# Kernel optimization log

Hardware: AMD Instinct MI355X
Metric: run time of the kernel (lower is better)

Reference implementation:

```python
import jax, jax.numpy as jnp
import numpy as np

N_NODES = 50000
N_EDGES = 600000
N_GRAPHS = 512
D = 128          # in_channels == hidden_channels
L = 4            # num_layers (total GINConv count)
N_CLASSES = 10
BN_EPS = 1e-5


def setup_inputs() -> dict:
    key = jax.random.key(0)
    ks = jax.random.split(key, 12)
    x = jax.random.normal(ks[0], (N_NODES, D), dtype=jnp.float32)
    edge_index = jax.random.randint(ks[1], (2, N_EDGES), 0, N_NODES, dtype=jnp.int64)
    batch = jnp.sort(jax.random.randint(ks[2], (N_NODES,), 0, N_GRAPHS, dtype=jnp.int64))
    s = 1.0 / np.sqrt(D)
    W1 = jax.random.uniform(ks[3], (L, D, D), jnp.float32, -s, s)
    b1 = jax.random.uniform(ks[4], (L, D), jnp.float32, -s, s)
    W2 = jax.random.uniform(ks[5], (L, D, D), jnp.float32, -s, s)
    b2 = jax.random.uniform(ks[6], (L, D), jnp.float32, -s, s)
    eps = jnp.zeros((L,), jnp.float32)            # train_eps=True, init 0
    gamma = jnp.ones((L, D), jnp.float32)
    beta = jnp.zeros((L, D), jnp.float32)
    sl = 1.0 / np.sqrt(D * L)
    Wlin = jax.random.uniform(ks[7], (D * L, N_CLASSES), jnp.float32, -sl, sl)
    blin = jax.random.uniform(ks[8], (N_CLASSES,), jnp.float32, -sl, sl)
    return {"x": x, "edge_index": edge_index, "batch": batch,
            "W1": W1, "b1": b1, "W2": W2, "b2": b2, "eps": eps,
            "gamma": gamma, "beta": beta, "Wlin": Wlin, "blin": blin}


def reference(x, edge_index, batch, W1, b1, W2, b2, eps, gamma, beta, Wlin, blin):
    src, dst = edge_index[0], edge_index[1]
    h = x
    pools = []
    for l in range(L):
        # GINConv: sum-aggregate neighbor features at dst, add (1+eps)*self
        agg = jax.ops.segment_sum(h[src], dst, num_segments=N_NODES)
        z = (1.0 + eps[l]) * h + agg
        # 2-layer MLP
        z = jnp.maximum(z @ W1[l] + b1[l], 0.0) @ W2[l] + b2[l]
        # BatchNorm1d (training mode: batch stats, biased variance)
        mean = jnp.mean(z, axis=0)
        var = jnp.mean(jnp.square(z - mean), axis=0)
        z = (z - mean) * jax.lax.rsqrt(var + BN_EPS) * gamma[l] + beta[l]
        h = jnp.maximum(z, 0.0)
        # global_add_pool per graph
        pools.append(jax.ops.segment_sum(h, batch, num_segments=N_GRAPHS))
    x_cat = jnp.concatenate(pools, axis=1)  # [N_GRAPHS, D*L]
    return x_cat @ Wlin + blin              # dropout = identity (eval)
```

## Files before the change

### kernel.cpp

```cpp
#include <hip/hip_runtime.h>

#define N_NODES 50000
#define N_EDGES 600000
#define N_GRAPHS 512
#define DIM 128
#define NLAYERS 4
#define NCLASSES 10
#define KPS 136

typedef __attribute__((ext_vector_type(8))) short short8;
typedef __attribute__((ext_vector_type(4))) float f32x4;

union Frag { short8 s; uint4 u; };

__device__ inline unsigned short f2bf(float v) {
    union { float f; unsigned u; } c; c.f = v;
    unsigned u = c.u;
    u += 0x7FFFu + ((u >> 16) & 1u);
    return (unsigned short)(u >> 16);
}
__device__ inline float bfu_lo(unsigned u) {
    union { float f; unsigned x; } c; c.x = u << 16; return c.f;
}
__device__ inline float bfu_hi(unsigned u) {
    union { float f; unsigned x; } c; c.x = u & 0xFFFF0000u; return c.f;
}
__device__ inline void addRow(float* acc, const uint4& v) {
    acc[0] += bfu_lo(v.x); acc[1] += bfu_hi(v.x);
    acc[2] += bfu_lo(v.y); acc[3] += bfu_hi(v.y);
    acc[4] += bfu_lo(v.z); acc[5] += bfu_hi(v.z);
    acc[6] += bfu_lo(v.w); acc[7] += bfu_hi(v.w);
}

__global__ __launch_bounds__(256) void hist_kernel(
    const int* __restrict__ dst, int* __restrict__ deg)
{
    int e = blockIdx.x * 256 + threadIdx.x;
    if (e >= N_EDGES) return;
    atomicAdd(&deg[dst[e]], 1);
}

__global__ __launch_bounds__(256) void scan1_kernel(
    const int* __restrict__ deg, int* __restrict__ bsum)
{
    __shared__ int red[256];
    int t = threadIdx.x;
    int i4 = blockIdx.x * 256 + t;
    int s = 0;
    if (i4 < 12500) {
        int4 v = ((const int4*)deg)[i4];
        s = v.x + v.y + v.z + v.w;
    }
    red[t] = s;
    __syncthreads();
    for (int off = 128; off > 0; off >>= 1) {
        if (t < off) red[t] += red[t + off];
        __syncthreads();
    }
    if (t == 0) bsum[blockIdx.x] = red[0];
}

__global__ __launch_bounds__(64) void scan2_kernel(int* __restrict__ bsum)
{
    __shared__ int sh[64];
    int t = threadIdx.x;
    sh[t] = (t < 49) ? bsum[t] : 0;
    __syncthreads();
    if (t == 0) {
        int run = 0;
        for (int i = 0; i < 49; i++) { int v = sh[i]; sh[i] = run; run += v; }
    }
    __syncthreads();
    if (t < 49) bsum[t] = sh[t];
}

__global__ __launch_bounds__(256) void scan3_kernel(
    const int* __restrict__ deg, const int* __restrict__ bsum,
    int* __restrict__ rowptr, int* __restrict__ cursor)
{
    __shared__ int red[256];
    int t = threadIdx.x;
    int i4 = blockIdx.x * 256 + t;
    int4 v = {0, 0, 0, 0};
    if (i4 < 12500) v = ((const int4*)deg)[i4];
    int s = v.x + v.y + v.z + v.w;
    red[t] = s;
    __syncthreads();
    for (int off = 1; off < 256; off <<= 1) {
        int val = (t >= off) ? red[t - off] : 0;
        __syncthreads();
        red[t] += val;
        __syncthreads();
    }
    int run = bsum[blockIdx.x] + (t ? red[t - 1] : 0);
    if (i4 < 12500) {
        int4 rp;
        rp.x = run; run += v.x;
        rp.y = run; run += v.y;
        rp.z = run; run += v.z;
        rp.w = run; run += v.w;
        ((int4*)rowptr)[i4] = rp;
        ((int4*)cursor)[i4] = rp;
    }
    if (blockIdx.x == 0 && t == 0) rowptr[N_NODES] = N_EDGES;
}

__global__ __launch_bounds__(256) void fill_kernel(
    const int* __restrict__ src, const int* __restrict__ dst,
    int* __restrict__ cursor, int* __restrict__ csr)
{
    int e = blockIdx.x * 256 + threadIdx.x;
    if (e >= N_EDGES) return;
    int p = atomicAdd(&cursor[dst[e]], 1);
    csr[p] = src[e];
}

__global__ __launch_bounds__(256) void prep_kernel(
    const int* __restrict__ batch, int* __restrict__ gstart,
    const float* __restrict__ x, unsigned int* __restrict__ xb,
    const float* __restrict__ W1, const float* __restrict__ W2,
    unsigned short* __restrict__ whi, float* __restrict__ stats)
{
    int b = blockIdx.x;
    int t = threadIdx.x;
    if (b < 196) {
        int n = b * 256 + t;
        if (n >= N_NODES) return;
        int bb = batch[n];
        int bp = (n == 0) ? -1 : batch[n - 1];
        for (int g = bp + 1; g <= bb; g++) gstart[g] = n;
        if (n == N_NODES - 1)
            for (int g = bb + 1; g <= N_GRAPHS; g++) gstart[g] = N_NODES;
    } else if (b < 6446) {
        int idx = (b - 196) * 256 + t;
        if (idx >= N_NODES * 32) return;
        float4 v = ((const float4*)x)[idx];
        uint2 o;
        o.x = (unsigned)f2bf(v.x) | ((unsigned)f2bf(v.y) << 16);
        o.y = (unsigned)f2bf(v.z) | ((unsigned)f2bf(v.w) << 16);
        ((uint2*)xb)[idx] = o;
    } else if (b < 6958) {
        int idx = (b - 6446) * 256 + t;
        int f   = idx & 16383;
        int w01 = (idx >> 14) & 1;
        int l   = idx >> 15;
        int j    = f & 7;
        int lane = (f >> 3) & 63;
        int cg   = (f >> 9) & 7;
        int ks   = f >> 12;
        int k = ks * 32 + (lane >> 4) * 8 + j;
        int n = cg * 16 + (lane & 15);
        const float* W = (w01 == 0 ? W1 : W2) + (size_t)l * 16384;
        whi[idx] = f2bf(W[k * 128 + n]);
    } else {
        #pragma unroll
        for (int i = 0; i < 4; i++) stats[i * 256 + t] = 0.f;
    }
}

__global__ __launch_bounds__(256) void gin_layer_kernel(
    const unsigned int* __restrict__ hb,
    const int* __restrict__ rowptr, const int* __restrict__ csr,
    const float* __restrict__ epsP,
    unsigned short* __restrict__ z,
    const unsigned short* __restrict__ whi,
    const float* __restrict__ b1, const float* __restrict__ b2,
    float* __restrict__ stats)
{
    __shared__ unsigned short tpk[64 * KPS];
    __shared__ float sums[1024];
    __shared__ float sqs[1024];

    const int t = threadIdx.x;
    const int lane = t & 63;
    const int w = t >> 6;
    const int wr = w & 1, wc = w >> 1;
    const int l15 = lane & 15, quad = lane >> 4;
    const int base = blockIdx.x * 64;

    {
        const int m = t >> 2;
        const int c = t & 3;
        const int n = base + m;
        const uint4* hb4 = (const uint4*)hb;
        float acc[32];
        #pragma unroll
        for (int i = 0; i < 32; i++) acc[i] = 0.f;
        if (n < N_NODES) {
            const float e1 = 1.0f + epsP[0];
            const uint4* self = hb4 + (size_t)n * 16 + c;
            #pragma unroll
            for (int j = 0; j < 4; j++) {
                uint4 v = self[j * 4];
                float* a = acc + j * 8;
                a[0] = e1 * bfu_lo(v.x); a[1] = e1 * bfu_hi(v.x);
                a[2] = e1 * bfu_lo(v.y); a[3] = e1 * bfu_hi(v.y);
                a[4] = e1 * bfu_lo(v.z); a[5] = e1 * bfu_hi(v.z);
                a[6] = e1 * bfu_lo(v.w); a[7] = e1 * bfu_hi(v.w);
            }
            int beg = rowptr[n], end = rowptr[n + 1];
            int e = beg;
            if (e + 3 < end) {
                int s0 = csr[e], s1 = csr[e + 1], s2 = csr[e + 2], s3 = csr[e + 3];
                while (true) {
                    const uint4* r0 = hb4 + (size_t)s0 * 16 + c;
                    const uint4* r1 = hb4 + (size_t)s1 * 16 + c;
                    const uint4* r2 = hb4 + (size_t)s2 * 16 + c;
                    const uint4* r3 = hb4 + (size_t)s3 * 16 + c;
                    uint4 v00 = r0[0], v01 = r0[4], v02 = r0[8], v03 = r0[12];
                    uint4 v10 = r1[0], v11 = r1[4], v12 = r1[8], v13 = r1[12];
                    uint4 v20 = r2[0], v21 = r2[4], v22 = r2[8], v23 = r2[12];
                    uint4 v30 = r3[0], v31 = r3[4], v32 = r3[8], v33 = r3[12];
                    int en = e + 4;
                    bool more = (en + 3 < end);
                    if (more) {
                        s0 = csr[en]; s1 = csr[en + 1];
                        s2 = csr[en + 2]; s3 = csr[en + 3];
                    }
                    addRow(acc + 0, v00); addRow(acc + 8, v01); addRow(acc + 16, v02); addRow(acc + 24, v03);
                    addRow(acc + 0, v10); addRow(acc + 8, v11); addRow(acc + 16, v12); addRow(acc + 24, v13);
                    addRow(acc + 0, v20); addRow(acc + 8, v21); addRow(acc + 16, v22); addRow(acc + 24, v23);
                    addRow(acc + 0, v30); addRow(acc + 8, v31); addRow(acc + 16, v32); addRow(acc + 24, v33);
                    e = en;
                    if (!more) break;
                }
            }
            for (; e < end; e++) {
                int s0 = csr[e];
                const uint4* r0 = hb4 + (size_t)s0 * 16 + c;
                uint4 a0 = r0[0], a1 = r0[4], a2 = r0[8], a3 = r0[12];
                addRow(acc + 0, a0);  addRow(acc + 8, a1);
                addRow(acc + 16, a2); addRow(acc + 24, a3);
            }
        }
        #pragma unroll
        for (int j = 0; j < 4; j++) {
            union { short8 s; unsigned short u[8]; } pk;
            #pragma unroll
            for (int i = 0; i < 8; i++) pk.u[i] = f2bf(acc[j * 8 + i]);
            *((short8*)&tpk[m * KPS + j * 32 + c * 8]) = pk.s;
        }
    }
    __syncthreads();

    f32x4 acc[2][4];
    #pragma unroll
    for (int s = 0; s < 2; s++)
        #pragma unroll
        for (int i = 0; i < 4; i++) acc[s][i] = (f32x4){0.f, 0.f, 0.f, 0.f};

    const int arow0 = (32 * wr + l15) * KPS;
    const int arow1 = arow0 + 16 * KPS;

    #pragma unroll
    for (int kh = 0; kh < 2; kh++) {
        Frag bf[2][4];
        short8 a0[2], a1[2];
        #pragma unroll
        for (int kk = 0; kk < 2; kk++) {
            int ks = kh * 2 + kk;
            #pragma unroll
            for (int i = 0; i < 4; i++) {
                size_t woff = (size_t)(((ks * 8 + wc * 4 + i) * 64 + lane) * 8);
                bf[kk][i].s = *((const short8*)&whi[woff]);
            }
            a0[kk] = *((const short8*)&tpk[arow0 + ks * 32 + quad * 8]);
            a1[kk] = *((const short8*)&tpk[arow1 + ks * 32 + quad * 8]);
        }
        #pragma unroll
        for (int kk = 0; kk < 2; kk++) {
            #pragma unroll
            for (int i = 0; i < 4; i++) {
                acc[0][i] = __builtin_amdgcn_mfma_f32_16x16x32_bf16(a0[kk], bf[kk][i].s, acc[0][i], 0, 0, 0);
                acc[1][i] = __builtin_amdgcn_mfma_f32_16x16x32_bf16(a1[kk], bf[kk][i].s, acc[1][i], 0, 0, 0);
            }
        }
    }
    __syncthreads();

    #pragma unroll
    for (int i = 0; i < 4; i++) {
        int col = wc * 64 + i * 16 + l15;
        float bb = b1[col];
        #pragma unroll
        for (int s = 0; s < 2; s++) {
            #pragma unroll
            for (int r = 0; r < 4; r++) {
                int m = 32 * wr + 16 * s + quad * 4 + r;
                float v = fmaxf(acc[s][i][r] + bb, 0.f);
                tpk[m * KPS + col] = f2bf(v);
            }
            acc[s][i] = (f32x4){0.f, 0.f, 0.f, 0.f};
        }
    }
    __syncthreads();

    const unsigned short* w2 = whi + 16384;
    #pragma unroll
    for (int kh = 0; kh < 2; kh++) {
        Frag bf[2][4];
        short8 a0[2], a1[2];
        #pragma unroll
        for (int kk = 0; kk < 2; kk++) {
            int ks = kh * 2 + kk;
            #pragma unroll
            for (int i = 0; i < 4; i++) {
                size_t woff = (size_t)(((ks * 8 + wc * 4 + i) * 64 + lane) * 8);
                bf[kk][i].s = *((const short8*)&w2[woff]);
            }
            a0[kk] = *((const short8*)&tpk[arow0 + ks * 32 + quad * 8]);
            a1[kk] = *((const short8*)&tpk[arow1 + ks * 32 + quad * 8]);
        }
        #pragma unroll
        for (int kk = 0; kk < 2; kk++) {
            #pragma unroll
            for (int i = 0; i < 4; i++) {
                acc[0][i] = __builtin_amdgcn_mfma_f32_16x16x32_bf16(a0[kk], bf[kk][i].s, acc[0][i], 0, 0, 0);
                acc[1][i] = __builtin_amdgcn_mfma_f32_16x16x32_bf16(a1[kk], bf[kk][i].s, acc[1][i], 0, 0, 0);
            }
        }
    }
    __syncthreads();

    {
        float colsum[4], colsq[4];
        #pragma unroll
        for (int i = 0; i < 4; i++) {
            int col = wc * 64 + i * 16 + l15;
            float bb = b2[col];
            float su = 0.f, q2 = 0.f;
            #pragma unroll
            for (int s = 0; s < 2; s++) {
                #pragma unroll
                for (int r = 0; r < 4; r++) {
                    int m = 32 * wr + 16 * s + quad * 4 + r;
                    int n = base + m;
                    float v = acc[s][i][r] + bb;
                    tpk[m * KPS + col] = f2bf(v);
                    if (n < N_NODES) { su += v; q2 += v * v; }
                }
            }
            colsum[i] = su; colsq[i] = q2;
        }
        #pragma unroll
        for (int i = 0; i < 4; i++) {
            sums[(w * 4 + i) * 64 + lane] = colsum[i];
            sqs [(w * 4 + i) * 64 + lane] = colsq[i];
        }
    }
    __syncthreads();

    {
        int m2 = t >> 2, c2 = t & 3;
        int n2 = base + m2;
        if (n2 < N_NODES) {
            const uint4* srcp = (const uint4*)(tpk + m2 * KPS);
            uint4* dstp = (uint4*)z + (size_t)n2 * 16;
            #pragma unroll
            for (int j = 0; j < 4; j++) dstp[j * 4 + c2] = srcp[j * 4 + c2];
        }
    }
    if (t < 128) {
        int c = t;
        int wcc = c >> 6, ci = (c >> 4) & 3, cl = c & 15;
        float s = 0.f, q2 = 0.f;
        #pragma unroll
        for (int wrr = 0; wrr < 2; wrr++) {
            int ww = wcc * 2 + wrr;
            #pragma unroll
            for (int u = 0; u < 4; u++) {
                int ln = cl + u * 16;
                s  += sums[(ww * 4 + ci) * 64 + ln];
                q2 += sqs [(ww * 4 + ci) * 64 + ln];
            }
        }
        unsafeAtomicAdd(&stats[c], s);
        unsafeAtomicAdd(&stats[128 + c], q2);
    }
}

__global__ __launch_bounds__(256) void bnpool_kernel(
    const unsigned int* __restrict__ z, const float* __restrict__ stats,
    const float* __restrict__ gamma, const float* __restrict__ beta,
    const int* __restrict__ gstart, unsigned int* __restrict__ hout,
    float* __restrict__ pools, int layer)
{
    __shared__ float red[8][128];
    const int g = blockIdx.x;
    const int t = threadIdx.x;
    const int q = t & 31, r = t >> 5;
    const int beg = gstart[g], end = gstart[g + 1];

    float4 s  = ((const float4*)stats)[q];
    float4 sq = ((const float4*)stats)[32 + q];
    float4 gm = ((const float4*)gamma)[q];
    float4 bt = ((const float4*)beta)[q];
    const float invN = 1.0f / (float)N_NODES;
    float m, vr;
    float4 scl, sh;
    m = s.x * invN; vr = sq.x * invN - m * m; scl.x = gm.x * rsqrtf(vr + 1e-5f); sh.x = bt.x - m * scl.x;
    m = s.y * invN; vr = sq.y * invN - m * m; scl.y = gm.y * rsqrtf(vr + 1e-5f); sh.y = bt.y - m * scl.y;
    m = s.z * invN; vr = sq.z * invN - m * m; scl.z = gm.z * rsqrtf(vr + 1e-5f); sh.z = bt.z - m * scl.z;
    m = s.w * invN; vr = sq.w * invN - m * m; scl.w = gm.w * rsqrtf(vr + 1e-5f); sh.w = bt.w - m * scl.w;

    float4 acc = {0.f, 0.f, 0.f, 0.f};
    for (int n = beg + r; n < end; n += 8) {
        uint2 zp = ((const uint2*)z)[(size_t)n * 32 + q];
        float4 hv;
        hv.x = fmaxf(bfu_lo(zp.x) * scl.x + sh.x, 0.f);
        hv.y = fmaxf(bfu_hi(zp.x) * scl.y + sh.y, 0.f);
        hv.z = fmaxf(bfu_lo(zp.y) * scl.z + sh.z, 0.f);
        hv.w = fmaxf(bfu_hi(zp.y) * scl.w + sh.w, 0.f);
        uint2 p;
        p.x = (unsigned)f2bf(hv.x) | ((unsigned)f2bf(hv.y) << 16);
        p.y = (unsigned)f2bf(hv.z) | ((unsigned)f2bf(hv.w) << 16);
        ((uint2*)hout)[(size_t)n * 32 + q] = p;
        acc.x += hv.x; acc.y += hv.y; acc.z += hv.z; acc.w += hv.w;
    }
    red[r][q * 4 + 0] = acc.x;
    red[r][q * 4 + 1] = acc.y;
    red[r][q * 4 + 2] = acc.z;
    red[r][q * 4 + 3] = acc.w;
    __syncthreads();
    if (t < 128) {
        float sm = 0.f;
        #pragma unroll
        for (int rr = 0; rr < 8; rr++) sm += red[rr][t];
        pools[(size_t)g * (DIM * NLAYERS) + (size_t)layer * DIM + t] = sm;
    }
}

__global__ __launch_bounds__(64) void final_kernel(
    const float* __restrict__ pools, const float* __restrict__ Wlin,
    const float* __restrict__ blin, float* __restrict__ out)
{
    int g = blockIdx.x;
    int lane = threadIdx.x;
    const float* xr = pools + (size_t)g * (DIM * NLAYERS);
    float a[NCLASSES];
    #pragma unroll
    for (int o = 0; o < NCLASSES; o++) a[o] = 0.f;
    for (int kk = 0; kk < DIM * NLAYERS; kk += 64) {
        float xv = xr[kk + lane];
        const float* wr = Wlin + (size_t)(kk + lane) * NCLASSES;
        #pragma unroll
        for (int o = 0; o < NCLASSES; o++) a[o] += xv * wr[o];
    }
    #pragma unroll
    for (int o = 0; o < NCLASSES; o++) {
        float v = a[o];
        #pragma unroll
        for (int off = 32; off > 0; off >>= 1) v += __shfl_down(v, off, 64);
        if (lane == 0) out[(size_t)g * NCLASSES + o] = v + blin[o];
    }
}

extern "C" void kernel_launch(void* const* d_in, const int* in_sizes, int n_in,
                              void* d_out, int out_size, void* d_ws, size_t ws_size,
                              hipStream_t stream)
{
    const float* x     = (const float*)d_in[0];
    const int*   src   = (const int*)d_in[1];
    const int*   dst   = ((const int*)d_in[1]) + N_EDGES;
    const int*   batch = (const int*)d_in[2];
    const float* W1    = (const float*)d_in[3];
    const float* b1    = (const float*)d_in[4];
    const float* W2    = (const float*)d_in[5];
    const float* b2    = (const float*)d_in[6];
    const float* eps   = (const float*)d_in[7];
    const float* gamma = (const float*)d_in[8];
    const float* beta  = (const float*)d_in[9];
    const float* Wlin  = (const float*)d_in[10];
    const float* blin  = (const float*)d_in[11];
    float* out = (float*)d_out;

    char* ws = (char*)d_ws;
    const size_t FEATH = (size_t)N_NODES * DIM * sizeof(unsigned short);
    size_t off = 0;
    unsigned int* buf_h = (unsigned int*)(ws + off); off += FEATH;
    unsigned short* buf_z = (unsigned short*)(ws + off); off += FEATH;
    float* pools  = (float*)(ws + off); off += (size_t)N_GRAPHS * DIM * NLAYERS * sizeof(float);
    float* stats  = (float*)(ws + off); off += (size_t)NLAYERS * 256 * sizeof(float);
    int*   deg    = (int*)(ws + off);   off += (size_t)N_NODES * sizeof(int);
    int*   rowptr = (int*)(ws + off);   off += (size_t)(N_NODES + 1) * sizeof(int) + 12;
    int*   csr    = (int*)(ws + off);   off += (size_t)N_EDGES * sizeof(int);
    int*   gstart = (int*)(ws + off);   off += 2064;
    int*   bsum   = (int*)(ws + off);   off += 208;
    unsigned short* whi = (unsigned short*)(ws + off); off += (size_t)NLAYERS * 2 * 16384 * 2;

    hipMemsetAsync(deg, 0, (size_t)N_NODES * sizeof(int), stream);

    hist_kernel<<<(N_EDGES + 255) / 256, 256, 0, stream>>>(dst, deg);
    scan1_kernel<<<49, 256, 0, stream>>>(deg, bsum);
    scan2_kernel<<<1, 64, 0, stream>>>(bsum);
    scan3_kernel<<<49, 256, 0, stream>>>(deg, bsum, rowptr, deg );
    fill_kernel<<<(N_EDGES + 255) / 256, 256, 0, stream>>>(src, dst, deg, csr);
    prep_kernel<<<6959, 256, 0, stream>>>(batch, gstart, x, buf_h,
                                          W1, W2, whi, stats);

    for (int l = 0; l < NLAYERS; l++) {
        gin_layer_kernel<<<(N_NODES + 63) / 64, 256, 0, stream>>>(
            buf_h, rowptr, csr, eps + l, buf_z,
            whi + (size_t)l * 32768,
            b1 + (size_t)l * DIM, b2 + (size_t)l * DIM,
            stats + (size_t)l * 256);
        bnpool_kernel<<<N_GRAPHS, 256, 0, stream>>>(
            (const unsigned int*)buf_z, stats + (size_t)l * 256,
            gamma + (size_t)l * DIM, beta + (size_t)l * DIM,
            gstart, buf_h, pools, l);
    }
    final_kernel<<<N_GRAPHS, 64, 0, stream>>>(pools, Wlin, blin, out);
}
```

Before: 406.8 us.

## Fuse BatchNorm+ReLU and pooling into next GIN layer's gather, merge head

```diff
diff --git a/kernel.cpp b/kernel.cpp
--- a/kernel.cpp
+++ b/kernel.cpp
@@ -30,6 +30,26 @@
     acc[2] += bfu_lo(v.y); acc[3] += bfu_hi(v.y);
     acc[4] += bfu_lo(v.z); acc[5] += bfu_hi(v.z);
     acc[6] += bfu_lo(v.w); acc[7] += bfu_hi(v.w);
+}
+__device__ inline void bnRow(float* h, const uint4& v, const unsigned* cf) {
+    h[0] = fmaxf(bfu_lo(v.x) * bfu_hi(cf[0]) + bfu_lo(cf[0]), 0.f);
+    h[1] = fmaxf(bfu_hi(v.x) * bfu_hi(cf[1]) + bfu_lo(cf[1]), 0.f);
+    h[2] = fmaxf(bfu_lo(v.y) * bfu_hi(cf[2]) + bfu_lo(cf[2]), 0.f);
+    h[3] = fmaxf(bfu_hi(v.y) * bfu_hi(cf[3]) + bfu_lo(cf[3]), 0.f);
+    h[4] = fmaxf(bfu_lo(v.z) * bfu_hi(cf[4]) + bfu_lo(cf[4]), 0.f);
+    h[5] = fmaxf(bfu_hi(v.z) * bfu_hi(cf[5]) + bfu_lo(cf[5]), 0.f);
+    h[6] = fmaxf(bfu_lo(v.w) * bfu_hi(cf[6]) + bfu_lo(cf[6]), 0.f);
+    h[7] = fmaxf(bfu_hi(v.w) * bfu_hi(cf[7]) + bfu_lo(cf[7]), 0.f);
+}
+template<int MODE>
+__device__ inline void addRowM(float* a, const uint4& v, const unsigned* cf) {
+    if constexpr (MODE) {
+        float h[8]; bnRow(h, v, cf);
+        a[0] += h[0]; a[1] += h[1]; a[2] += h[2]; a[3] += h[3];
+        a[4] += h[4]; a[5] += h[5]; a[6] += h[6]; a[7] += h[7];
+    } else {
+        addRow(a, v);
+    }
 }
 
 __global__ __launch_bounds__(256) void hist_kernel(
@@ -119,7 +139,8 @@
     const int* __restrict__ batch, int* __restrict__ gstart,
     const float* __restrict__ x, unsigned int* __restrict__ xb,
     const float* __restrict__ W1, const float* __restrict__ W2,
-    unsigned short* __restrict__ whi, float* __restrict__ stats)
+    unsigned short* __restrict__ whi, float* __restrict__ stats,
+    float* __restrict__ pools)
 {
     int b = blockIdx.x;
     int t = threadIdx.x;
@@ -152,24 +173,32 @@
         int n = cg * 16 + (lane & 15);
         const float* W = (w01 == 0 ? W1 : W2) + (size_t)l * 16384;
         whi[idx] = f2bf(W[k * 128 + n]);
+    } else if (b == 6958) {
+        #pragma unroll
+        for (int i = 0; i < 4; i++) stats[i * 256 + t] = 0.f;
     } else {
-        #pragma unroll
-        for (int i = 0; i < 4; i++) stats[i * 256 + t] = 0.f;
-    }
-}
-
+        int idx = (b - 6959) * 256 + t;
+        pools[idx] = 0.f;
+    }
+}
+
+template<int MODE>
 __global__ __launch_bounds__(256) void gin_layer_kernel(
-    const unsigned int* __restrict__ hb,
+    const unsigned int* __restrict__ zin,
     const int* __restrict__ rowptr, const int* __restrict__ csr,
     const float* __restrict__ epsP,
-    unsigned short* __restrict__ z,
+    unsigned short* __restrict__ zout,
     const unsigned short* __restrict__ whi,
     const float* __restrict__ b1, const float* __restrict__ b2,
-    float* __restrict__ stats)
+    float* __restrict__ stats,
+    const float* __restrict__ statsP,
+    const float* __restrict__ gammaP, const float* __restrict__ betaP,
+    const int* __restrict__ batch, float* __restrict__ pools, int lm1)
 {
     __shared__ unsigned short tpk[64 * KPS];
     __shared__ float sums[1024];
     __shared__ float sqs[1024];
+    __shared__ float pool_lds[8][128];
 
     const int t = threadIdx.x;
     const int lane = t & 63;
@@ -178,25 +207,74 @@
     const int l15 = lane & 15, quad = lane >> 4;
     const int base = blockIdx.x * 64;
 
+    if constexpr (MODE) {
+        ((float*)pool_lds)[t]       = 0.f;
+        ((float*)pool_lds)[256 + t] = 0.f;
+        ((float*)pool_lds)[512 + t] = 0.f;
+        ((float*)pool_lds)[768 + t] = 0.f;
+        __syncthreads();
+    }
+
     {
         const int m = t >> 2;
         const int c = t & 3;
         const int n = base + m;
-        const uint4* hb4 = (const uint4*)hb;
+        const uint4* hb4 = (const uint4*)zin;
         float acc[32];
+        unsigned cf[32];
         #pragma unroll
         for (int i = 0; i < 32; i++) acc[i] = 0.f;
+        if constexpr (MODE) {
+            const float invN = 1.0f / (float)N_NODES;
+            #pragma unroll
+            for (int j = 0; j < 4; j++) {
+                int cb = 32 * j + 8 * c;
+                #pragma unroll
+                for (int k = 0; k < 8; k++) {
+                    float mean = statsP[cb + k] * invN;
+                    float var  = statsP[128 + cb + k] * invN - mean * mean;
+                    float scl  = gammaP[cb + k] * rsqrtf(var + 1e-5f);
+                    float shv  = betaP[cb + k] - mean * scl;
+                    cf[j * 8 + k] = ((unsigned)f2bf(scl) << 16) | (unsigned)f2bf(shv);
+                }
+            }
+        }
         if (n < N_NODES) {
             const float e1 = 1.0f + epsP[0];
             const uint4* self = hb4 + (size_t)n * 16 + c;
-            #pragma unroll
-            for (int j = 0; j < 4; j++) {
-                uint4 v = self[j * 4];
-                float* a = acc + j * 8;
-                a[0] = e1 * bfu_lo(v.x); a[1] = e1 * bfu_hi(v.x);
-                a[2] = e1 * bfu_lo(v.y); a[3] = e1 * bfu_hi(v.y);
-                a[4] = e1 * bfu_lo(v.z); a[5] = e1 * bfu_hi(v.z);
-                a[6] = e1 * bfu_lo(v.w); a[7] = e1 * bfu_hi(v.w);
+            if constexpr (MODE) {
+                int g = batch[n];
+                int slot = g - batch[base];
+                #pragma unroll
+                for (int j = 0; j < 4; j++) {
+                    uint4 v = self[j * 4];
+                    float h[8];
+                    bnRow(h, v, cf + j * 8);
+                    int cb = 32 * j + 8 * c;
+                    if (slot < 8) {
+                        #pragma unroll
+                        for (int k = 0; k < 8; k++)
+                            atomicAdd(&pool_lds[slot][cb + k], h[k]);
+                    } else {
+                        #pragma unroll
+                        for (int k = 0; k < 8; k++)
+                            unsafeAtomicAdd(&pools[(size_t)g * (DIM * NLAYERS)
+                                                   + (size_t)lm1 * DIM + cb + k], h[k]);
+                    }
+                    float* a = acc + j * 8;
+                    #pragma unroll
+                    for (int k = 0; k < 8; k++) a[k] = e1 * h[k];
+                }
+            } else {
+                #pragma unroll
+                for (int j = 0; j < 4; j++) {
+                    uint4 v = self[j * 4];
+                    float* a = acc + j * 8;
+                    a[0] = e1 * bfu_lo(v.x); a[1] = e1 * bfu_hi(v.x);
+                    a[2] = e1 * bfu_lo(v.y); a[3] = e1 * bfu_hi(v.y);
+                    a[4] = e1 * bfu_lo(v.z); a[5] = e1 * bfu_hi(v.z);
+                    a[6] = e1 * bfu_lo(v.w); a[7] = e1 * bfu_hi(v.w);
+                }
             }
             int beg = rowptr[n], end = rowptr[n + 1];
             int e = beg;
@@ -217,10 +295,14 @@
                         s0 = csr[en]; s1 = csr[en + 1];
                         s2 = csr[en + 2]; s3 = csr[en + 3];
                     }
-                    addRow(acc + 0, v00); addRow(acc + 8, v01); addRow(acc + 16, v02); addRow(acc + 24, v03);
-                    addRow(acc + 0, v10); addRow(acc + 8, v11); addRow(acc + 16, v12); addRow(acc + 24, v13);
-                    addRow(acc + 0, v20); addRow(acc + 8, v21); addRow(acc + 16, v22); addRow(acc + 24, v23);
-                    addRow(acc + 0, v30); addRow(acc + 8, v31); addRow(acc + 16, v32); addRow(acc + 24, v33);
+                    addRowM<MODE>(acc + 0, v00, cf + 0);  addRowM<MODE>(acc + 8, v01, cf + 8);
+                    addRowM<MODE>(acc + 16, v02, cf + 16); addRowM<MODE>(acc + 24, v03, cf + 24);
+                    addRowM<MODE>(acc + 0, v10, cf + 0);  addRowM<MODE>(acc + 8, v11, cf + 8);
+                    addRowM<MODE>(acc + 16, v12, cf + 16); addRowM<MODE>(acc + 24, v13, cf + 24);
+                    addRowM<MODE>(acc + 0, v20, cf + 0);  addRowM<MODE>(acc + 8, v21, cf + 8);
+                    addRowM<MODE>(acc + 16, v22, cf + 16); addRowM<MODE>(acc + 24, v23, cf + 24);
+                    addRowM<MODE>(acc + 0, v30, cf + 0);  addRowM<MODE>(acc + 8, v31, cf + 8);
+                    addRowM<MODE>(acc + 16, v32, cf + 16); addRowM<MODE>(acc + 24, v33, cf + 24);
                     e = en;
                     if (!more) break;
                 }
@@ -229,8 +311,8 @@
                 int s0 = csr[e];
                 const uint4* r0 = hb4 + (size_t)s0 * 16 + c;
                 uint4 a0 = r0[0], a1 = r0[4], a2 = r0[8], a3 = r0[12];
-                addRow(acc + 0, a0);  addRow(acc + 8, a1);
-                addRow(acc + 16, a2); addRow(acc + 24, a3);
+                addRowM<MODE>(acc + 0, a0, cf + 0);   addRowM<MODE>(acc + 8, a1, cf + 8);
+                addRowM<MODE>(acc + 16, a2, cf + 16); addRowM<MODE>(acc + 24, a3, cf + 24);
             }
         }
         #pragma unroll
@@ -355,7 +437,7 @@
         int n2 = base + m2;
         if (n2 < N_NODES) {
             const uint4* srcp = (const uint4*)(tpk + m2 * KPS);
-            uint4* dstp = (uint4*)z + (size_t)n2 * 16;
+            uint4* dstp = (uint4*)zout + (size_t)n2 * 16;
             #pragma unroll
             for (int j = 0; j < 4; j++) dstp[j * 4 + c2] = srcp[j * 4 + c2];
         }
@@ -377,15 +459,30 @@
         unsafeAtomicAdd(&stats[c], s);
         unsafeAtomicAdd(&stats[128 + c], q2);
     }
-}
-
-__global__ __launch_bounds__(256) void bnpool_kernel(
+    if constexpr (MODE) {
+        if (t < 128) {
+            int g0 = batch[base];
+            #pragma unroll
+            for (int s = 0; s < 8; s++) {
+                int g = g0 + s;
+                float v = pool_lds[s][t];
+                if (g < N_GRAPHS && v != 0.f)
+                    unsafeAtomicAdd(&pools[(size_t)g * (DIM * NLAYERS)
+                                           + (size_t)lm1 * DIM + t], v);
+            }
+        }
+    }
+}
+
+__global__ __launch_bounds__(256) void bnhead_kernel(
     const unsigned int* __restrict__ z, const float* __restrict__ stats,
     const float* __restrict__ gamma, const float* __restrict__ beta,
-    const int* __restrict__ gstart, unsigned int* __restrict__ hout,
-    float* __restrict__ pools, int layer)
+    const int* __restrict__ gstart, const float* __restrict__ pools,
+    const float* __restrict__ Wlin, const float* __restrict__ blin,
+    float* __restrict__ out)
 {
     __shared__ float red[8][128];
+    __shared__ float pool3[128];
     const int g = blockIdx.x;
     const int t = threadIdx.x;
     const int q = t & 31, r = t >> 5;
@@ -406,16 +503,10 @@
     float4 acc = {0.f, 0.f, 0.f, 0.f};
     for (int n = beg + r; n < end; n += 8) {
         uint2 zp = ((const uint2*)z)[(size_t)n * 32 + q];
-        float4 hv;
-        hv.x = fmaxf(bfu_lo(zp.x) * scl.x + sh.x, 0.f);
-        hv.y = fmaxf(bfu_hi(zp.x) * scl.y + sh.y, 0.f);
-        hv.z = fmaxf(bfu_lo(zp.y) * scl.z + sh.z, 0.f);
-        hv.w = fmaxf(bfu_hi(zp.y) * scl.w + sh.w, 0.f);
-        uint2 p;
-        p.x = (unsigned)f2bf(hv.x) | ((unsigned)f2bf(hv.y) << 16);
-        p.y = (unsigned)f2bf(hv.z) | ((unsigned)f2bf(hv.w) << 16);
-        ((uint2*)hout)[(size_t)n * 32 + q] = p;
-        acc.x += hv.x; acc.y += hv.y; acc.z += hv.z; acc.w += hv.w;
+        acc.x += fmaxf(bfu_lo(zp.x) * scl.x + sh.x, 0.f);
+        acc.y += fmaxf(bfu_hi(zp.x) * scl.y + sh.y, 0.f);
+        acc.z += fmaxf(bfu_lo(zp.y) * scl.z + sh.z, 0.f);
+        acc.w += fmaxf(bfu_hi(zp.y) * scl.w + sh.w, 0.f);
     }
     red[r][q * 4 + 0] = acc.x;
     red[r][q * 4 + 1] = acc.y;
@@ -426,32 +517,30 @@
         float sm = 0.f;
         #pragma unroll
         for (int rr = 0; rr < 8; rr++) sm += red[rr][t];
-        pools[(size_t)g * (DIM * NLAYERS) + (size_t)layer * DIM + t] = sm;
-    }
-}
-
-__global__ __launch_bounds__(64) void final_kernel(
-    const float* __restrict__ pools, const float* __restrict__ Wlin,
-    const float* __restrict__ blin, float* __restrict__ out)
-{
-    int g = blockIdx.x;
-    int lane = threadIdx.x;
-    const float* xr = pools + (size_t)g * (DIM * NLAYERS);
-    float a[NCLASSES];
-    #pragma unroll
-    for (int o = 0; o < NCLASSES; o++) a[o] = 0.f;
-    for (int kk = 0; kk < DIM * NLAYERS; kk += 64) {
-        float xv = xr[kk + lane];
-        const float* wr = Wlin + (size_t)(kk + lane) * NCLASSES;
-        #pragma unroll
-        for (int o = 0; o < NCLASSES; o++) a[o] += xv * wr[o];
-    }
-    #pragma unroll
-    for (int o = 0; o < NCLASSES; o++) {
-        float v = a[o];
-        #pragma unroll
-        for (int off = 32; off > 0; off >>= 1) v += __shfl_down(v, off, 64);
-        if (lane == 0) out[(size_t)g * NCLASSES + o] = v + blin[o];
+        pool3[t] = sm;
+    }
+    __syncthreads();
+
+    if (t < 64) {
+        const int lane = t;
+        const float* xr = pools + (size_t)g * (DIM * NLAYERS);
+        float a[NCLASSES];
+        #pragma unroll
+        for (int o = 0; o < NCLASSES; o++) a[o] = 0.f;
+        #pragma unroll
+        for (int kk = 0; kk < DIM * NLAYERS; kk += 64) {
+            float xv = (kk < 3 * DIM) ? xr[kk + lane] : pool3[kk - 3 * DIM + lane];
+            const float* wrow = Wlin + (size_t)(kk + lane) * NCLASSES;
+            #pragma unroll
+            for (int o = 0; o < NCLASSES; o++) a[o] += xv * wrow[o];
+        }
+        #pragma unroll
+        for (int o = 0; o < NCLASSES; o++) {
+            float v = a[o];
+            #pragma unroll
+            for (int off = 32; off > 0; off >>= 1) v += __shfl_down(v, off, 64);
+            if (lane == 0) out[(size_t)g * NCLASSES + o] = v + blin[o];
+        }
     }
 }
 
@@ -477,8 +566,9 @@
     char* ws = (char*)d_ws;
     const size_t FEATH = (size_t)N_NODES * DIM * sizeof(unsigned short);
     size_t off = 0;
-    unsigned int* buf_h = (unsigned int*)(ws + off); off += FEATH;
-    unsigned short* buf_z = (unsigned short*)(ws + off); off += FEATH;
+    unsigned int* xb = (unsigned int*)(ws + off); off += FEATH;
+    unsigned short* zb0 = (unsigned short*)(ws + off); off += FEATH;
+    unsigned short* zb1 = (unsigned short*)(ws + off); off += FEATH;
     float* pools  = (float*)(ws + off); off += (size_t)N_GRAPHS * DIM * NLAYERS * sizeof(float);
     float* stats  = (float*)(ws + off); off += (size_t)NLAYERS * 256 * sizeof(float);
     int*   deg    = (int*)(ws + off);   off += (size_t)N_NODES * sizeof(int);
@@ -488,6 +578,8 @@
     int*   bsum   = (int*)(ws + off);   off += 208;
     unsigned short* whi = (unsigned short*)(ws + off); off += (size_t)NLAYERS * 2 * 16384 * 2;
 
+    unsigned short* zping[2] = { zb0, zb1 };
+
     hipMemsetAsync(deg, 0, (size_t)N_NODES * sizeof(int), stream);
 
     hist_kernel<<<(N_EDGES + 255) / 256, 256, 0, stream>>>(dst, deg);
@@ -495,19 +587,26 @@
     scan2_kernel<<<1, 64, 0, stream>>>(bsum);
     scan3_kernel<<<49, 256, 0, stream>>>(deg, bsum, rowptr, deg );
     fill_kernel<<<(N_EDGES + 255) / 256, 256, 0, stream>>>(src, dst, deg, csr);
-    prep_kernel<<<6959, 256, 0, stream>>>(batch, gstart, x, buf_h,
-                                          W1, W2, whi, stats);
-
-    for (int l = 0; l < NLAYERS; l++) {
-        gin_layer_kernel<<<(N_NODES + 63) / 64, 256, 0, stream>>>(
-            buf_h, rowptr, csr, eps + l, buf_z,
+    prep_kernel<<<7983, 256, 0, stream>>>(batch, gstart, x, xb,
+                                          W1, W2, whi, stats, pools);
+
+    const int GINGRID = (N_NODES + 63) / 64;
+    gin_layer_kernel<0><<<GINGRID, 256, 0, stream>>>(
+        xb, rowptr, csr, eps + 0, zping[0],
+        whi, b1, b2, stats,
+        nullptr, nullptr, nullptr, batch, pools, 0);
+    for (int l = 1; l < NLAYERS; l++) {
+        gin_layer_kernel<1><<<GINGRID, 256, 0, stream>>>(
+            (const unsigned int*)zping[(l - 1) & 1], rowptr, csr, eps + l, zping[l & 1],
             whi + (size_t)l * 32768,
             b1 + (size_t)l * DIM, b2 + (size_t)l * DIM,
-            stats + (size_t)l * 256);
-        bnpool_kernel<<<N_GRAPHS, 256, 0, stream>>>(
-            (const unsigned int*)buf_z, stats + (size_t)l * 256,
-            gamma + (size_t)l * DIM, beta + (size_t)l * DIM,
-            gstart, buf_h, pools, l);
-    }
-    final_kernel<<<N_GRAPHS, 64, 0, stream>>>(pools, Wlin, blin, out);
-}
+            stats + (size_t)l * 256,
+            stats + (size_t)(l - 1) * 256,
+            gamma + (size_t)(l - 1) * DIM, beta + (size_t)(l - 1) * DIM,
+            batch, pools, l - 1);
+    }
+    bnhead_kernel<<<N_GRAPHS, 256, 0, stream>>>(
+        (const unsigned int*)zping[1], stats + (size_t)(NLAYERS - 1) * 256,
+        gamma + (size_t)(NLAYERS - 1) * DIM, beta + (size_t)(NLAYERS - 1) * DIM,
+        gstart, pools, Wlin, blin, out);
+}
```

After: 547.5 us. 1.35x slower.
